# Performance work log

Hardware: AMD Instinct MI355X
Metric: run time of the kernel (lower is better)

Reference implementation:

```python
import math
import jax, jax.numpy as jnp
import numpy as np

NUM_EXPERTS = 8
CAPACITY_FACTOR = 1.5

def setup_inputs() -> dict:
    key = jax.random.key(0)
    ks = jax.random.split(key, 4)
    B, T, D, F, E = 4, 2048, 1024, 4096, NUM_EXPERTS
    scale = 0.02
    return {
        "x": jax.random.normal(ks[0], (B, T, D), dtype=jnp.float32),
        "router_w": jax.random.normal(ks[1], (E, D), dtype=jnp.float32) * scale,  # nn.Linear(D,E,bias=False).weight
        "w1": jax.random.normal(ks[2], (E, D, F), dtype=jnp.float32) * scale,
        "b1": jnp.zeros((E, F), dtype=jnp.float32),
        "w2": jax.random.normal(ks[3], (E, F, D), dtype=jnp.float32) * scale,
        "b2": jnp.zeros((E, D), dtype=jnp.float32),
    }

def reference(x, router_w, w1, b1, w2, b2):
    B, T, D = x.shape
    E = router_w.shape[0]
    N = B * T
    C = max(math.ceil(CAPACITY_FACTOR * N / E), 1)  # static per-expert capacity

    x_flat = x.reshape(N, D)
    logits = x_flat @ router_w.T                      # [N, E]
    probs = jax.nn.softmax(logits, axis=-1)
    chosen_e = jnp.argmax(probs, axis=-1)             # [N] int
    chosen_p = jnp.max(probs, axis=-1)                # [N]

    # First-come-first-served capacity: position of each token within its expert's queue
    onehot = jax.nn.one_hot(chosen_e, E, dtype=jnp.float32)          # [N, E]
    pos = jnp.take_along_axis(jnp.cumsum(onehot, axis=0), chosen_e[:, None], axis=1)[:, 0] - 1.0
    pos = pos.astype(jnp.int32)                                       # [N]
    kept = (pos < C)                                                  # [N] bool
    pos_c = jnp.clip(pos, 0, C - 1)

    # Scatter tokens into per-expert capacity buffers [E, C, D]; dropped tokens contribute 0
    buf = jnp.zeros((E, C, D), dtype=x.dtype).at[chosen_e, pos_c].add(
        x_flat * kept[:, None].astype(x.dtype))

    # Expert FFN: Linear -> exact GELU -> Linear (torch nn.GELU default = erf)
    h = jax.nn.gelu(jnp.einsum('ecd,edf->ecf', buf, w1) + b1[:, None, :], approximate=False)
    eo = jnp.einsum('ecf,efd->ecd', h, w2) + b2[:, None, :]           # [E, C, D]

    # Gather back and scale by router prob; dropped tokens get zeros
    y = eo[chosen_e, pos_c] * (chosen_p * kept.astype(x.dtype))[:, None]
    return y.reshape(B, T, D)
```

## Files before the change

### kernel.cpp

```cpp
#include <hip/hip_runtime.h>
#include <hip/hip_bf16.h>
#include <math.h>

typedef unsigned short u16;
typedef __attribute__((ext_vector_type(8))) short short8;
typedef __attribute__((ext_vector_type(4))) float f32x4;

#define NTOK 8192
#define DMODEL 1024
#define FDIM 4096
#define NEXP 8
#define CAP 1536

__device__ __forceinline__ u16 f2bf(float f) {
  __hip_bfloat16 b = __float2bfloat16(f);
  u16 u;
  __builtin_memcpy(&u, &b, 2);
  return u;
}

__device__ __forceinline__ float gelu_exact(float v) {
  float x = v * 0.70710678118654752f;
  float ax = fabsf(x);
  float t = __builtin_amdgcn_rcpf(1.0f + 0.3275911f * ax);
  float p =
      t * (0.254829592f +
           t * (-0.284496736f +
                t * (1.421413741f + t * (-1.453152027f + t * 1.061405429f))));
  float er = 1.0f - p * __expf(-ax * ax);
  er = copysignf(er, x);
  return 0.5f * v * (1.0f + er);
}

__device__ __forceinline__ void gload_lds16(const u16* g, u16* l) {
  __builtin_amdgcn_global_load_lds(
      (const __attribute__((address_space(1))) void*)g,
      (__attribute__((address_space(3))) void*)l, 16, 0, 0);
}

__global__ __launch_bounds__(256) void router_cast_kernel(
    const float* __restrict__ x, const float* __restrict__ rw,
    u16* __restrict__ xbf, int* __restrict__ chosen_e,
    float* __restrict__ chosen_p) {
  int b = blockIdx.x, tid = threadIdx.x;
  if (b < 4096) {
    size_t base = (size_t)b * 2048 + tid * 8;
    float4 v0 = *(const float4*)(x + base);
    float4 v1 = *(const float4*)(x + base + 4);
    short8 sv;
    sv[0] = (short)f2bf(v0.x); sv[1] = (short)f2bf(v0.y);
    sv[2] = (short)f2bf(v0.z); sv[3] = (short)f2bf(v0.w);
    sv[4] = (short)f2bf(v1.x); sv[5] = (short)f2bf(v1.y);
    sv[6] = (short)f2bf(v1.z); sv[7] = (short)f2bf(v1.w);
    *(short8*)(xbf + base) = sv;
  } else {
    int tok = ((b - 4096) * 256 + tid) >> 6;
    int lane = tid & 63;
    const float4* xp = (const float4*)(x + (size_t)tok * DMODEL) + lane * 4;
    float4 x0 = xp[0], x1 = xp[1], x2 = xp[2], x3 = xp[3];
    float l[8];
#pragma unroll
    for (int e = 0; e < 8; e++) {
      const float4* wp = (const float4*)(rw + (size_t)e * DMODEL) + lane * 4;
      float4 w0 = wp[0], w1v = wp[1], w2v = wp[2], w3 = wp[3];
      float s = x0.x * w0.x + x0.y * w0.y + x0.z * w0.z + x0.w * w0.w;
      s += x1.x * w1v.x + x1.y * w1v.y + x1.z * w1v.z + x1.w * w1v.w;
      s += x2.x * w2v.x + x2.y * w2v.y + x2.z * w2v.z + x2.w * w2v.w;
      s += x3.x * w3.x + x3.y * w3.y + x3.z * w3.z + x3.w * w3.w;
      l[e] = s;
    }
#pragma unroll
    for (int off = 32; off > 0; off >>= 1) {
#pragma unroll
      for (int e = 0; e < 8; e++) l[e] += __shfl_xor(l[e], off, 64);
    }
    if (lane == 0) {
      float best = l[0];
      int am = 0;
#pragma unroll
      for (int e = 1; e < 8; e++)
        if (l[e] > best) { best = l[e]; am = e; }
      float denom = 0.f;
#pragma unroll
      for (int e = 0; e < 8; e++) denom += expf(l[e] - best);
      chosen_e[tok] = am;
      chosen_p[tok] = 1.0f / denom;
    }
  }
}

__device__ __forceinline__ void trans256(const float* __restrict__ ip,
                                         u16* __restrict__ op, int Rin,
                                         int Cin, int r0, int c0, char* lds,
                                         int tid) {
  int w = tid >> 6, l = tid & 63;
#pragma unroll
  for (int i = 0; i < 16; i++) {
    int row = w * 16 + i;
    float4 v = *(const float4*)(ip + (size_t)(r0 + row) * Cin + c0 + l * 4);
    uint2 d;
    d.x = (unsigned)f2bf(v.x) | ((unsigned)f2bf(v.y) << 16);
    d.y = (unsigned)f2bf(v.z) | ((unsigned)f2bf(v.w) << 16);
    int ch = (l >> 1) ^ ((row >> 3) & 7);
    *(uint2*)(lds + row * 512 + ch * 16 + (l & 1) * 8) = d;
  }
  __syncthreads();
#pragma unroll
  for (int p = 0; p < 2; p++) {
    int c = ((tid >> 5) + p * 32) * 4;
    int rb = (tid & 31) * 8;
    short8 s0, s1, s2, s3;
#pragma unroll
    for (int j = 0; j < 8; j++) {
      int r = rb + j;
      int ch = (c >> 3) ^ ((r >> 3) & 7);
      uint2 d = *(const uint2*)(lds + r * 512 + ch * 16 + (c & 7) * 2);
      s0[j] = (short)(d.x & 0xffff);
      s1[j] = (short)(d.x >> 16);
      s2[j] = (short)(d.y & 0xffff);
      s3[j] = (short)(d.y >> 16);
    }
    u16* ob = op + (size_t)(c0 + c) * Rin + r0 + rb;
    *(short8*)(ob) = s0;
    *(short8*)(ob + (size_t)Rin) = s1;
    *(short8*)(ob + 2 * (size_t)Rin) = s2;
    *(short8*)(ob + 3 * (size_t)Rin) = s3;
  }
}

__global__ __launch_bounds__(1024, 1) void wtrans_kernel(
    const float* __restrict__ w1, const float* __restrict__ w2,
    u16* __restrict__ w1t, u16* __restrict__ w2t,
    const int* __restrict__ chosen_e, int* __restrict__ tok_of_slot,
    int* __restrict__ counts, float* __restrict__ out) {
  extern __shared__ char lds[];
  int b = blockIdx.x, tid = threadIdx.x;
  if (b == 0) {
    if (tid < 512) {
      int w = tid >> 6, lane = tid & 63;
      unsigned long long ltmask =
          (lane == 63) ? ~0ull >> 1 : (1ull << lane) - 1ull;
      int cnt = 0;
      for (int c = 0; c < NTOK / 64; c++) {
        int i = c * 64 + lane;
        int e = chosen_e[i];
        unsigned long long bal = __ballot(e == w);
        if (e == w) {
          int p = cnt + __popcll(bal & ltmask);
          if (p < CAP) {
            tok_of_slot[w * CAP + p] = i;
          } else {
            float4 z = make_float4(0.f, 0.f, 0.f, 0.f);
            float* orow = out + (size_t)i * DMODEL;
            for (int d = 0; d < DMODEL; d += 4) *(float4*)(orow + d) = z;
          }
        }
        cnt += __popcll(bal);
      }
      for (int p = cnt + lane; p < CAP; p += 64) tok_of_slot[w * CAP + p] = -1;
      if (lane == 0) counts[w] = cnt < CAP ? cnt : CAP;
    }
  } else if (b < 513) {
    int idx = b - 1;
    int e = idx >> 6, rem = idx & 63;
    int r0 = (rem >> 4) * 256, c0 = (rem & 15) * 256;
    trans256(w1 + (size_t)e * DMODEL * FDIM, w1t + (size_t)e * DMODEL * FDIM,
             DMODEL, FDIM, r0, c0, lds, tid);
  } else {
    int idx = b - 513;
    int e = idx >> 6, rem = idx & 63;
    int r0 = (rem >> 2) * 256, c0 = (rem & 3) * 256;
    trans256(w2 + (size_t)e * DMODEL * FDIM, w2t + (size_t)e * DMODEL * FDIM,
             FDIM, DMODEL, r0, c0, lds, tid);
  }
}

template <int NX, int NY>
__device__ __forceinline__ void tile_coords(int& bx, int& by, int& bz) {
  int flat = blockIdx.x + NX * (blockIdx.y + NY * blockIdx.z);
  int nwg = NX * NY * (int)gridDim.z;
  int swz = (flat & 7) * (nwg >> 3) + (flat >> 3);
  bx = swz % NX;
  int rem = swz / NX;
  by = rem % NY;
  bz = rem / NY;
}

template <int KD>
__device__ __forceinline__ void mainloop_db(const u16* pa0, const u16* pa1,
                                            const u16* pb0, const u16* pb1,
                                            u16* smem, f32x4 (&acc)[4][4],
                                            int tid) {
  int wid = tid >> 6, lane = tid & 63;
  int wm = (wid >> 1) * 64, wn = (wid & 1) * 64;
  int fr = lane & 15, fk = (lane >> 4) * 8;
  int aro = (wm + fr) * 32 + fk;
  int bro = 4096 + (wn + fr) * 32 + fk;
  gload_lds16(pa0, smem + tid * 8);
  gload_lds16(pa1, smem + 2048 + tid * 8);
  gload_lds16(pb0, smem + 4096 + tid * 8);
  gload_lds16(pb1, smem + 6144 + tid * 8);
  __syncthreads();
  int cur = 0;
#pragma unroll 1
  for (int t = 0; t < KD / 32; ++t) {
    const u16* cb = smem + cur * 8192;
    u16* nb = smem + (cur ^ 1) * 8192;
    if (t + 1 < KD / 32) {
      int k = (t + 1) * 32;
      gload_lds16(pa0 + k, nb + tid * 8);
      gload_lds16(pa1 + k, nb + 2048 + tid * 8);
      gload_lds16(pb0 + k, nb + 4096 + tid * 8);
      gload_lds16(pb1 + k, nb + 6144 + tid * 8);
    }
    short8 av[4], bv[4];
#pragma unroll
    for (int m = 0; m < 4; m++) av[m] = *(const short8*)(cb + aro + m * 512);
#pragma unroll
    for (int n = 0; n < 4; n++) bv[n] = *(const short8*)(cb + bro + n * 512);
#pragma unroll
    for (int m = 0; m < 4; m++)
#pragma unroll
      for (int n = 0; n < 4; n++)
        acc[m][n] = __builtin_amdgcn_mfma_f32_16x16x32_bf16(av[m], bv[n],
                                                            acc[m][n], 0, 0, 0);
    __syncthreads();
    cur ^= 1;
  }
}

#define VMWAIT(N) asm volatile("s_waitcnt vmcnt(" #N ")" ::: "memory")
#define LGKM0 asm volatile("s_waitcnt lgkmcnt(0)" ::: "memory")

#define G1_STAGE_A(t)                                              \
  {                                                                \
    u16* d_ = smem + ((t) & 3) * 16384 + tid * 8;                  \
    gload_lds16(pa0 + (t) * 32, d_);                               \
    gload_lds16(pa1 + (t) * 32, d_ + 4096);                        \
  }
#define G1_STAGE_B(t)                                              \
  {                                                                \
    u16* d_ = smem + ((t) & 3) * 16384 + 8192 + tid * 8;           \
    gload_lds16(pb0 + (t) * 32, d_);                               \
    gload_lds16(pb1 + (t) * 32, d_ + 4096);                        \
  }

#define G1_TILE(t, VMSTMT, DO_ISSUE)                                          \
  {                                                                           \
    const u16* Ab_ = smem + ((t) & 3) * 16384;                                \
    short8 a_[8], b0_, b1_;                                                   \
    _Pragma("unroll") for (int m_ = 0; m_ < 8; m_++) a_[m_] =                 \
        *(const short8*)(Ab_ + aoff + m_ * 512);                              \
    b0_ = *(const short8*)(Ab_ + boff);                                       \
    b1_ = *(const short8*)(Ab_ + boff + 512);                                 \
    if (DO_ISSUE) G1_STAGE_A((t) + 3);                                        \
    __builtin_amdgcn_s_barrier();                                             \
    LGKM0;                                                                    \
    __builtin_amdgcn_s_setprio(1);                                            \
    _Pragma("unroll") for (int m_ = 0; m_ < 8; m_++) {                        \
      acc[m_][0] = __builtin_amdgcn_mfma_f32_16x16x32_bf16(a_[m_], b0_,       \
                                                           acc[m_][0], 0, 0,  \
                                                           0);                \
      acc[m_][1] = __builtin_amdgcn_mfma_f32_16x16x32_bf16(a_[m_], b1_,       \
                                                           acc[m_][1], 0, 0,  \
                                                           0);                \
    }                                                                         \
    __builtin_amdgcn_s_setprio(0);                                            \
    __builtin_amdgcn_s_barrier();                                             \
    short8 b2_ = *(const short8*)(Ab_ + boff + 1024);                         \
    short8 b3_ = *(const short8*)(Ab_ + boff + 1536);                         \
    if (DO_ISSUE) G1_STAGE_B((t) + 3);                                        \
    VMSTMT;                                                                   \
    __builtin_amdgcn_s_barrier();                                             \
    LGKM0;                                                                    \
    __builtin_amdgcn_s_setprio(1);                                            \
    _Pragma("unroll") for (int m_ = 0; m_ < 8; m_++) {                        \
      acc[m_][2] = __builtin_amdgcn_mfma_f32_16x16x32_bf16(a_[m_], b2_,       \
                                                           acc[m_][2], 0, 0,  \
                                                           0);                \
      acc[m_][3] = __builtin_amdgcn_mfma_f32_16x16x32_bf16(a_[m_], b3_,       \
                                                           acc[m_][3], 0, 0,  \
                                                           0);                \
    }                                                                         \
    __builtin_amdgcn_s_setprio(0);                                            \
    __builtin_amdgcn_s_barrier();                                             \
  }

template <int NX, int NY>
__global__ __launch_bounds__(512, 2) void gemm1_kernel(
    const u16* __restrict__ xbf, const u16* __restrict__ w1tB,
    const int* __restrict__ tok_of_slot, const int* __restrict__ counts,
    u16* __restrict__ hB, const float* __restrict__ b1, int e0,
    long long hStrideE) {
  extern __shared__ __align__(16) u16 smem[];
  int bx, by, bz;
  tile_coords<NX, NY>(bx, by, bz);
  int e = e0 + bz;
  int m0 = by * 256, n0 = bx * 256;
  if (m0 >= counts[e]) return;
  const u16* Bg = w1tB + (size_t)e * FDIM * DMODEL;
  u16* H = hB + (size_t)bz * hStrideE;
  int tid = threadIdx.x;

  int r4 = tid >> 2, c8 = (tid & 3) * 8;
  int t0 = tok_of_slot[e * CAP + m0 + r4];
  t0 &= ~(t0 >> 31);
  int t1 = tok_of_slot[e * CAP + m0 + 128 + r4];
  t1 &= ~(t1 >> 31);
  const u16* pa0 = xbf + (size_t)t0 * DMODEL + c8;
  const u16* pa1 = xbf + (size_t)t1 * DMODEL + c8;
  const u16* pb0 = Bg + (size_t)(n0 + r4) * DMODEL + c8;
  const u16* pb1 = pb0 + (size_t)128 * DMODEL;

  int wid = tid >> 6, lane = tid & 63;
  int wm = (wid >> 2) * 128, wn = (wid & 3) * 64;
  int fr = lane & 15, fk = (lane >> 4) * 8;
  int aoff = (wm + fr) * 32 + fk;
  int boff = 8192 + (wn + fr) * 32 + fk;
  f32x4 acc[8][4] = {};

  G1_STAGE_A(0); G1_STAGE_B(0);
  G1_STAGE_A(1); G1_STAGE_B(1);
  G1_STAGE_A(2); G1_STAGE_B(2);
  VMWAIT(8);
  __builtin_amdgcn_s_barrier();

  const int KT = DMODEL / 32;
#pragma unroll 1
  for (int t = 0; t < KT - 3; ++t) G1_TILE(t, VMWAIT(8), true);
  G1_TILE(KT - 3, VMWAIT(4), false);
  G1_TILE(KT - 2, VMWAIT(0), false);
  G1_TILE(KT - 1, (void)0, false);

  int fq = lane >> 4;
  const float* b1g = b1 + (size_t)e * FDIM + n0;
  float bias[4];
#pragma unroll
  for (int n = 0; n < 4; n++) bias[n] = b1g[wn + n * 16 + fr];
#pragma unroll
  for (int m = 0; m < 8; m++) {
#pragma unroll
    for (int n = 0; n < 4; n++) {
      int colL = wn + n * 16 + fr;
#pragma unroll
      for (int j = 0; j < 4; j++) {
        int rL = wm + m * 16 + fq * 4 + j;
        float v = gelu_exact(acc[m][n][j] + bias[n]);
        int ch = (colL >> 3) ^ ((rL >> 2) & 7);
        smem[rL * 256 + ch * 8 + (colL & 7)] = f2bf(v);
      }
    }
  }
  __syncthreads();
#pragma unroll
  for (int p = 0; p < 16; p++) {
    int idx = p * 512 + tid;
    int rr = idx >> 5, cch = idx & 31;
    int ch = cch ^ ((rr >> 2) & 7);
    short8 v = *(const short8*)(smem + rr * 256 + ch * 8);
    *(short8*)(H + (size_t)(m0 + rr) * FDIM + n0 + cch * 8) = v;
  }
}

template <int NX, int NY>
__global__ __launch_bounds__(256) void gemm2_kernel(
    const u16* __restrict__ hB, const u16* __restrict__ w2tB,
    float* __restrict__ out, const float* __restrict__ b2,
    const int* __restrict__ tok_of_slot, const int* __restrict__ counts,
    const float* __restrict__ chosen_p, int e0, long long hStrideE) {
  __shared__ __align__(16) u16 smem[16384];
  int bx, by, bz;
  tile_coords<NX, NY>(bx, by, bz);
  int e = e0 + bz;
  int m0 = by * 128, n0 = bx * 128;
  if (m0 >= counts[e]) return;
  const u16* Ag = hB + (size_t)bz * hStrideE;
  const u16* Bg = w2tB + (size_t)e * DMODEL * FDIM;
  const float* b2g = b2 + (size_t)e * DMODEL;
  int tid = threadIdx.x;
  int r2 = tid >> 2, c8 = (tid & 3) * 8;
  const u16* pa0 = Ag + (size_t)(m0 + r2) * FDIM + c8;
  const u16* pa1 = pa0 + (size_t)64 * FDIM;
  const u16* pb0 = Bg + (size_t)(n0 + r2) * FDIM + c8;
  const u16* pb1 = pb0 + (size_t)64 * FDIM;
  f32x4 acc[4][4] = {};
  mainloop_db<FDIM>(pa0, pa1, pb0, pb1, smem, acc, tid);

  int wid = tid >> 6, lane = tid & 63;
  int wm = (wid >> 1) * 64, wn = (wid & 1) * 64;
  int fr = lane & 15, fq = lane >> 4;
  float bias[4];
#pragma unroll
  for (int n = 0; n < 4; n++) bias[n] = b2g[n0 + wn + n * 16 + fr];
#pragma unroll
  for (int m = 0; m < 4; m++) {
#pragma unroll
    for (int j = 0; j < 4; j++) {
      int rL = wm + m * 16 + fq * 4 + j;
      int tk = tok_of_slot[e * CAP + m0 + rL];
      if (tk >= 0) {
        float sc = chosen_p[tk];
#pragma unroll
        for (int n = 0; n < 4; n++) {
          int colL = wn + n * 16 + fr;
          out[(size_t)tk * DMODEL + n0 + colL] = (acc[m][n][j] + bias[n]) * sc;
        }
      }
    }
  }
}

extern "C" void kernel_launch(void* const* d_in, const int* in_sizes, int n_in,
                              void* d_out, int out_size, void* d_ws,
                              size_t ws_size, hipStream_t stream) {
  const float* x = (const float*)d_in[0];
  const float* rw = (const float*)d_in[1];
  const float* w1 = (const float*)d_in[2];
  const float* b1 = (const float*)d_in[3];
  const float* w2 = (const float*)d_in[4];
  const float* b2 = (const float*)d_in[5];
  float* out = (float*)d_out;

  char* ws = (char*)d_ws;
  size_t off = 0;
  auto alloc = [&](size_t bytes) -> void* {
    void* p = ws + off;
    off = (off + bytes + 255) & ~(size_t)255;
    return p;
  };
  int* chosen_e = (int*)alloc((size_t)NTOK * 4);
  float* chosen_p = (float*)alloc((size_t)NTOK * 4);
  int* tok_of_slot = (int*)alloc((size_t)NEXP * CAP * 4);
  int* counts = (int*)alloc(NEXP * 4);
  u16* xbf = (u16*)alloc((size_t)NTOK * DMODEL * 2);
  u16* w1t = (u16*)alloc((size_t)NEXP * DMODEL * FDIM * 2);
  u16* w2t = (u16*)alloc((size_t)NEXP * DMODEL * FDIM * 2);
  size_t hFull = (size_t)NEXP * CAP * FDIM * 2;
  size_t hLoop = (size_t)CAP * FDIM * 2;
  bool full = (off + hFull) <= ws_size;
  u16* h = (u16*)alloc(full ? hFull : hLoop);

  static_assert(CAP % 256 == 0 && FDIM % 256 == 0 && DMODEL % 128 == 0, "");
  const int TLDS = 131072, G1LDS = 131072;
  hipFuncSetAttribute((const void*)wtrans_kernel,
                      hipFuncAttributeMaxDynamicSharedMemorySize, TLDS);
  hipFuncSetAttribute((const void*)gemm1_kernel<FDIM / 256, CAP / 256>,
                      hipFuncAttributeMaxDynamicSharedMemorySize, G1LDS);

  router_cast_kernel<<<4096 + NTOK / 4, 256, 0, stream>>>(x, rw, xbf, chosen_e,
                                                          chosen_p);
  wtrans_kernel<<<1025, 1024, TLDS, stream>>>(w1, w2, w1t, w2t, chosen_e,
                                              tok_of_slot, counts, out);

  if (full) {
    gemm1_kernel<FDIM / 256, CAP / 256>
        <<<dim3(FDIM / 256, CAP / 256, NEXP), 512, G1LDS, stream>>>(
            xbf, w1t, tok_of_slot, counts, h, b1, 0, (long long)CAP * FDIM);
    gemm2_kernel<DMODEL / 128, CAP / 128>
        <<<dim3(DMODEL / 128, CAP / 128, NEXP), 256, 0, stream>>>(
            h, w2t, out, b2, tok_of_slot, counts, chosen_p, 0,
            (long long)CAP * FDIM);
  } else {
    for (int e = 0; e < NEXP; e++) {
      gemm1_kernel<FDIM / 256, CAP / 256>
          <<<dim3(FDIM / 256, CAP / 256, 1), 512, G1LDS, stream>>>(
              xbf, w1t, tok_of_slot, counts, h, b1, e, 0);
      gemm2_kernel<DMODEL / 128, CAP / 128>
          <<<dim3(DMODEL / 128, CAP / 128, 1), 256, 0, stream>>>(
              h, w2t, out, b2, tok_of_slot, counts, chosen_p, e, 0);
    }
  }
  (void)in_sizes;
  (void)n_in;
  (void)ws_size;
}
```

Baseline: 333.3 us.

## Gather tokens into contiguous expert buffers and tile weight layout by k-panels

Replaces the full-x bf16 cast with a gather kernel that writes each expert's capacity slots contiguously in bf16, so gemm1 loads A rows from contiguous memory instead of indirecting through tok_of_slot. The transposed weights are now stored in 32-wide k-panels, so each k-step of the B operand reads one contiguous block rather than strided rows. This aims to improve load coalescing and locality in both GEMMs, at the cost of an extra kernel launch and a larger gathered activation buffer.

```diff
diff --git a/kernel.cpp b/kernel.cpp
--- a/kernel.cpp
+++ b/kernel.cpp
@@ -38,54 +38,41 @@
       (__attribute__((address_space(3))) void*)l, 16, 0, 0);
 }
 
-__global__ __launch_bounds__(256) void router_cast_kernel(
+__global__ __launch_bounds__(256) void router_kernel(
     const float* __restrict__ x, const float* __restrict__ rw,
-    u16* __restrict__ xbf, int* __restrict__ chosen_e,
-    float* __restrict__ chosen_p) {
+    int* __restrict__ chosen_e, float* __restrict__ chosen_p) {
   int b = blockIdx.x, tid = threadIdx.x;
-  if (b < 4096) {
-    size_t base = (size_t)b * 2048 + tid * 8;
-    float4 v0 = *(const float4*)(x + base);
-    float4 v1 = *(const float4*)(x + base + 4);
-    short8 sv;
-    sv[0] = (short)f2bf(v0.x); sv[1] = (short)f2bf(v0.y);
-    sv[2] = (short)f2bf(v0.z); sv[3] = (short)f2bf(v0.w);
-    sv[4] = (short)f2bf(v1.x); sv[5] = (short)f2bf(v1.y);
-    sv[6] = (short)f2bf(v1.z); sv[7] = (short)f2bf(v1.w);
-    *(short8*)(xbf + base) = sv;
-  } else {
-    int tok = ((b - 4096) * 256 + tid) >> 6;
-    int lane = tid & 63;
-    const float4* xp = (const float4*)(x + (size_t)tok * DMODEL) + lane * 4;
-    float4 x0 = xp[0], x1 = xp[1], x2 = xp[2], x3 = xp[3];
-    float l[8];
-#pragma unroll
-    for (int e = 0; e < 8; e++) {
-      const float4* wp = (const float4*)(rw + (size_t)e * DMODEL) + lane * 4;
-      float4 w0 = wp[0], w1v = wp[1], w2v = wp[2], w3 = wp[3];
-      float s = x0.x * w0.x + x0.y * w0.y + x0.z * w0.z + x0.w * w0.w;
-      s += x1.x * w1v.x + x1.y * w1v.y + x1.z * w1v.z + x1.w * w1v.w;
-      s += x2.x * w2v.x + x2.y * w2v.y + x2.z * w2v.z + x2.w * w2v.w;
-      s += x3.x * w3.x + x3.y * w3.y + x3.z * w3.z + x3.w * w3.w;
-      l[e] = s;
-    }
-#pragma unroll
-    for (int off = 32; off > 0; off >>= 1) {
-#pragma unroll
-      for (int e = 0; e < 8; e++) l[e] += __shfl_xor(l[e], off, 64);
-    }
-    if (lane == 0) {
-      float best = l[0];
-      int am = 0;
-#pragma unroll
-      for (int e = 1; e < 8; e++)
-        if (l[e] > best) { best = l[e]; am = e; }
-      float denom = 0.f;
-#pragma unroll
-      for (int e = 0; e < 8; e++) denom += expf(l[e] - best);
-      chosen_e[tok] = am;
-      chosen_p[tok] = 1.0f / denom;
-    }
+  int tok = (b * 256 + tid) >> 6;
+  int lane = tid & 63;
+  const float4* xp = (const float4*)(x + (size_t)tok * DMODEL) + lane * 4;
+  float4 x0 = xp[0], x1 = xp[1], x2 = xp[2], x3 = xp[3];
+  float l[8];
+#pragma unroll
+  for (int e = 0; e < 8; e++) {
+    const float4* wp = (const float4*)(rw + (size_t)e * DMODEL) + lane * 4;
+    float4 w0 = wp[0], w1v = wp[1], w2v = wp[2], w3 = wp[3];
+    float s = x0.x * w0.x + x0.y * w0.y + x0.z * w0.z + x0.w * w0.w;
+    s += x1.x * w1v.x + x1.y * w1v.y + x1.z * w1v.z + x1.w * w1v.w;
+    s += x2.x * w2v.x + x2.y * w2v.y + x2.z * w2v.z + x2.w * w2v.w;
+    s += x3.x * w3.x + x3.y * w3.y + x3.z * w3.z + x3.w * w3.w;
+    l[e] = s;
+  }
+#pragma unroll
+  for (int off = 32; off > 0; off >>= 1) {
+#pragma unroll
+    for (int e = 0; e < 8; e++) l[e] += __shfl_xor(l[e], off, 64);
+  }
+  if (lane == 0) {
+    float best = l[0];
+    int am = 0;
+#pragma unroll
+    for (int e = 1; e < 8; e++)
+      if (l[e] > best) { best = l[e]; am = e; }
+    float denom = 0.f;
+#pragma unroll
+    for (int e = 0; e < 8; e++) denom += expf(l[e] - best);
+    chosen_e[tok] = am;
+    chosen_p[tok] = 1.0f / denom;
   }
 }
 
@@ -120,11 +107,12 @@
       s2[j] = (short)(d.y & 0xffff);
       s3[j] = (short)(d.y >> 16);
     }
-    u16* ob = op + (size_t)(c0 + c) * Rin + r0 + rb;
+    u16* ob = op + (size_t)((r0 + rb) >> 5) * Cin * 32 +
+              (size_t)(c0 + c) * 32 + ((r0 + rb) & 31);
     *(short8*)(ob) = s0;
-    *(short8*)(ob + (size_t)Rin) = s1;
-    *(short8*)(ob + 2 * (size_t)Rin) = s2;
-    *(short8*)(ob + 3 * (size_t)Rin) = s3;
+    *(short8*)(ob + 32) = s1;
+    *(short8*)(ob + 64) = s2;
+    *(short8*)(ob + 96) = s3;
   }
 }
 
@@ -175,6 +163,34 @@
   }
 }
 
+__global__ __launch_bounds__(256) void gather_kernel(
+    const float* __restrict__ x, const int* __restrict__ tok_of_slot,
+    u16* __restrict__ xg) {
+  int slot = blockIdx.x * 4 + (threadIdx.x >> 6);
+  int lane = threadIdx.x & 63;
+  int tok = tok_of_slot[slot];
+  u16* dst = xg + (size_t)slot * DMODEL + lane * 16;
+  if (tok < 0) {
+    short8 z = {};
+    *(short8*)(dst) = z;
+    *(short8*)(dst + 8) = z;
+    return;
+  }
+  const float4* sp = (const float4*)(x + (size_t)tok * DMODEL) + lane * 4;
+  float4 a = sp[0], b = sp[1], c = sp[2], d = sp[3];
+  short8 s0, s1;
+  s0[0] = (short)f2bf(a.x); s0[1] = (short)f2bf(a.y);
+  s0[2] = (short)f2bf(a.z); s0[3] = (short)f2bf(a.w);
+  s0[4] = (short)f2bf(b.x); s0[5] = (short)f2bf(b.y);
+  s0[6] = (short)f2bf(b.z); s0[7] = (short)f2bf(b.w);
+  s1[0] = (short)f2bf(c.x); s1[1] = (short)f2bf(c.y);
+  s1[2] = (short)f2bf(c.z); s1[3] = (short)f2bf(c.w);
+  s1[4] = (short)f2bf(d.x); s1[5] = (short)f2bf(d.y);
+  s1[6] = (short)f2bf(d.z); s1[7] = (short)f2bf(d.w);
+  *(short8*)(dst) = s0;
+  *(short8*)(dst + 8) = s1;
+}
+
 template <int NX, int NY>
 __device__ __forceinline__ void tile_coords(int& bx, int& by, int& bz) {
   int flat = blockIdx.x + NX * (blockIdx.y + NY * blockIdx.z);
@@ -189,8 +205,8 @@
 template <int KD>
 __device__ __forceinline__ void mainloop_db(const u16* pa0, const u16* pa1,
                                             const u16* pb0, const u16* pb1,
-                                            u16* smem, f32x4 (&acc)[4][4],
-                                            int tid) {
+                                            size_t bstep, u16* smem,
+                                            f32x4 (&acc)[4][4], int tid) {
   int wid = tid >> 6, lane = tid & 63;
   int wm = (wid >> 1) * 64, wn = (wid & 1) * 64;
   int fr = lane & 15, fk = (lane >> 4) * 8;
@@ -207,11 +223,10 @@
     const u16* cb = smem + cur * 8192;
     u16* nb = smem + (cur ^ 1) * 8192;
     if (t + 1 < KD / 32) {
-      int k = (t + 1) * 32;
-      gload_lds16(pa0 + k, nb + tid * 8);
-      gload_lds16(pa1 + k, nb + 2048 + tid * 8);
-      gload_lds16(pb0 + k, nb + 4096 + tid * 8);
-      gload_lds16(pb1 + k, nb + 6144 + tid * 8);
+      gload_lds16(pa0 + (t + 1) * 32, nb + tid * 8);
+      gload_lds16(pa1 + (t + 1) * 32, nb + 2048 + tid * 8);
+      gload_lds16(pb0 + (size_t)(t + 1) * bstep, nb + 4096 + tid * 8);
+      gload_lds16(pb1 + (size_t)(t + 1) * bstep, nb + 6144 + tid * 8);
     }
     short8 av[4], bv[4];
 #pragma unroll
@@ -241,8 +256,8 @@
 #define G1_STAGE_B(t)                                              \
   {                                                                \
     u16* d_ = smem + ((t) & 3) * 16384 + 8192 + tid * 8;           \
-    gload_lds16(pb0 + (t) * 32, d_);                               \
-    gload_lds16(pb1 + (t) * 32, d_ + 4096);                        \
+    gload_lds16(pb0 + (size_t)(t) * (FDIM * 32), d_);              \
+    gload_lds16(pb1 + (size_t)(t) * (FDIM * 32), d_ + 4096);       \
   }
 
 #define G1_TILE(t, VMSTMT, DO_ISSUE)                                          \
@@ -288,10 +303,9 @@
 
 template <int NX, int NY>
 __global__ __launch_bounds__(512, 2) void gemm1_kernel(
-    const u16* __restrict__ xbf, const u16* __restrict__ w1tB,
-    const int* __restrict__ tok_of_slot, const int* __restrict__ counts,
-    u16* __restrict__ hB, const float* __restrict__ b1, int e0,
-    long long hStrideE) {
+    const u16* __restrict__ xg, const u16* __restrict__ w1tB,
+    const int* __restrict__ counts, u16* __restrict__ hB,
+    const float* __restrict__ b1, int e0, long long hStrideE) {
   extern __shared__ __align__(16) u16 smem[];
   int bx, by, bz;
   tile_coords<NX, NY>(bx, by, bz);
@@ -303,14 +317,10 @@
   int tid = threadIdx.x;
 
   int r4 = tid >> 2, c8 = (tid & 3) * 8;
-  int t0 = tok_of_slot[e * CAP + m0 + r4];
-  t0 &= ~(t0 >> 31);
-  int t1 = tok_of_slot[e * CAP + m0 + 128 + r4];
-  t1 &= ~(t1 >> 31);
-  const u16* pa0 = xbf + (size_t)t0 * DMODEL + c8;
-  const u16* pa1 = xbf + (size_t)t1 * DMODEL + c8;
-  const u16* pb0 = Bg + (size_t)(n0 + r4) * DMODEL + c8;
-  const u16* pb1 = pb0 + (size_t)128 * DMODEL;
+  const u16* pa0 = xg + (size_t)(e * CAP + m0 + r4) * DMODEL + c8;
+  const u16* pa1 = pa0 + (size_t)128 * DMODEL;
+  const u16* pb0 = Bg + (size_t)(n0 + r4) * 32 + c8;
+  const u16* pb1 = pb0 + 128 * 32;
 
   int wid = tid >> 6, lane = tid & 63;
   int wm = (wid >> 2) * 128, wn = (wid & 3) * 64;
@@ -381,10 +391,10 @@
   int r2 = tid >> 2, c8 = (tid & 3) * 8;
   const u16* pa0 = Ag + (size_t)(m0 + r2) * FDIM + c8;
   const u16* pa1 = pa0 + (size_t)64 * FDIM;
-  const u16* pb0 = Bg + (size_t)(n0 + r2) * FDIM + c8;
-  const u16* pb1 = pb0 + (size_t)64 * FDIM;
+  const u16* pb0 = Bg + (size_t)(n0 + r2) * 32 + c8;
+  const u16* pb1 = pb0 + 64 * 32;
   f32x4 acc[4][4] = {};
-  mainloop_db<FDIM>(pa0, pa1, pb0, pb1, smem, acc, tid);
+  mainloop_db<FDIM>(pa0, pa1, pb0, pb1, (size_t)DMODEL * 32, smem, acc, tid);
 
   int wid = tid >> 6, lane = tid & 63;
   int wm = (wid >> 1) * 64, wn = (wid & 1) * 64;
@@ -432,7 +442,7 @@
   float* chosen_p = (float*)alloc((size_t)NTOK * 4);
   int* tok_of_slot = (int*)alloc((size_t)NEXP * CAP * 4);
   int* counts = (int*)alloc(NEXP * 4);
-  u16* xbf = (u16*)alloc((size_t)NTOK * DMODEL * 2);
+  u16* xg = (u16*)alloc((size_t)NEXP * CAP * DMODEL * 2);
   u16* w1t = (u16*)alloc((size_t)NEXP * DMODEL * FDIM * 2);
   u16* w2t = (u16*)alloc((size_t)NEXP * DMODEL * FDIM * 2);
   size_t hFull = (size_t)NEXP * CAP * FDIM * 2;
@@ -447,15 +457,15 @@
   hipFuncSetAttribute((const void*)gemm1_kernel<FDIM / 256, CAP / 256>,
                       hipFuncAttributeMaxDynamicSharedMemorySize, G1LDS);
 
-  router_cast_kernel<<<4096 + NTOK / 4, 256, 0, stream>>>(x, rw, xbf, chosen_e,
-                                                          chosen_p);
+  router_kernel<<<NTOK / 4, 256, 0, stream>>>(x, rw, chosen_e, chosen_p);
   wtrans_kernel<<<1025, 1024, TLDS, stream>>>(w1, w2, w1t, w2t, chosen_e,
                                               tok_of_slot, counts, out);
+  gather_kernel<<<NEXP * CAP / 4, 256, 0, stream>>>(x, tok_of_slot, xg);
 
   if (full) {
     gemm1_kernel<FDIM / 256, CAP / 256>
         <<<dim3(FDIM / 256, CAP / 256, NEXP), 512, G1LDS, stream>>>(
-            xbf, w1t, tok_of_slot, counts, h, b1, 0, (long long)CAP * FDIM);
+            xg, w1t, counts, h, b1, 0, (long long)CAP * FDIM);
     gemm2_kernel<DMODEL / 128, CAP / 128>
         <<<dim3(DMODEL / 128, CAP / 128, NEXP), 256, 0, stream>>>(
             h, w2t, out, b2, tok_of_slot, counts, chosen_p, 0,
@@ -464,7 +474,7 @@
     for (int e = 0; e < NEXP; e++) {
       gemm1_kernel<FDIM / 256, CAP / 256>
           <<<dim3(FDIM / 256, CAP / 256, 1), 512, G1LDS, stream>>>(
-              xbf, w1t, tok_of_slot, counts, h, b1, e, 0);
+              xg, w1t, counts, h, b1, e, 0);
       gemm2_kernel<DMODEL / 128, CAP / 128>
           <<<dim3(DMODEL / 128, CAP / 128, 1), 256, 0, stream>>>(
               h, w2t, out, b2, tok_of_slot, counts, chosen_p, e, 0);
```

After: 354.6 us. 1.06x slower.
